# Performance work log

Hardware: AMD Instinct MI355X
Metric: run time of the kernel (lower is better)

Reference implementation:

```python
import jax, jax.numpy as jnp
import numpy as np

B, LQ, LK = 1, 2048, 2048
D, H, KVH, DH = 4096, 32, 8, 128
G = H // KVH  # head groups


def setup_inputs() -> dict:
    key = jax.random.key(0)
    ks = jax.random.split(key, 7)
    s = 0.02
    hidden_q = jax.random.normal(ks[0], (B, LQ, D), dtype=jnp.float32)
    hidden_kv = jax.random.normal(ks[1], (B, LK, D), dtype=jnp.float32)
    # causal boolean mask (batch, len_q, len_k)
    attention_mask = jnp.broadcast_to(jnp.tril(jnp.ones((LQ, LK), dtype=bool)), (B, LQ, LK))
    position_bias = jax.random.normal(ks[2], (H, LQ, LK), dtype=jnp.float32) * 0.1
    Wq = jax.random.normal(ks[3], (D, H * DH), dtype=jnp.float32) * s
    Wk = jax.random.normal(ks[4], (D, KVH * DH), dtype=jnp.float32) * s
    Wv = jax.random.normal(ks[5], (D, KVH * DH), dtype=jnp.float32) * s
    Wo = jax.random.normal(ks[6], (H * DH, D), dtype=jnp.float32) * s
    return {"hidden_q": hidden_q, "hidden_kv": hidden_kv,
            "attention_mask": attention_mask, "position_bias": position_bias,
            "Wq": Wq, "Wk": Wk, "Wv": Wv, "Wo": Wo}


def reference(hidden_q, hidden_kv, attention_mask, position_bias, Wq, Wk, Wv, Wo):
    inv4 = DH ** -0.25  # q and k each scaled by dim_head**-1/4
    q = (hidden_q @ Wq) * inv4            # [B, LQ, H*DH]
    k = (hidden_kv @ Wk) * inv4           # [B, LK, KVH*DH]
    v = hidden_kv @ Wv                     # [B, LK, KVH*DH]
    q = q.reshape(B, LQ, KVH, G, DH)       # group heads for GQA
    k = k.reshape(B, LK, KVH, DH)
    v = v.reshape(B, LK, KVH, DH)
    # score: [B, KVH, G, LQ, LK] -> [B, H, LQ, LK]
    score = jnp.einsum('bqkgd,blkd->bkgql', q, k).reshape(B, H, LQ, LK)
    score = score + position_bias[None]
    mask = attention_mask[:, None]         # [B, 1, LQ, LK]
    score = jnp.where(mask, score, -jnp.inf)
    p = jax.nn.softmax(score, axis=-1)
    p = jnp.where(mask, p, 0.0)
    out = jnp.einsum('bkgql,blkd->bqkgd', p.reshape(B, KVH, G, LQ, LK), v)
    out = out.reshape(B, LQ, H * DH) @ Wo  # [B, LQ, D]
    return out
```

## Files before the change

kernel.cpp:

```cpp
#include <hip/hip_runtime.h>
#include <hip/hip_bf16.h>
#include <cstdint>
#include <cstddef>

typedef __attribute__((ext_vector_type(4))) float f32x4;
typedef __attribute__((ext_vector_type(4))) short s16x4;
typedef __attribute__((ext_vector_type(8))) short s16x8;

#define SLQ 2048
#define SLK 2048
#define SNH 32
#define SDH 128
#define LOG2E 1.4426950408889634f

__device__ __forceinline__ short f2bf(float x) {
  unsigned u = __builtin_bit_cast(unsigned, x);
  u += 0x7FFF + ((u >> 16) & 1);
  return (short)(u >> 16);
}

__device__ __forceinline__ void gload_lds16(const void* g, const void* l) {
  __builtin_amdgcn_global_load_lds((const __attribute__((address_space(1))) void*)g,
                                   (__attribute__((address_space(3))) void*)l,
                                   16, 0, 0);
}

template<int CTRL>
__device__ __forceinline__ float dpp_f32(float x) {
  return __builtin_bit_cast(float, __builtin_amdgcn_update_dpp(
      0, __builtin_bit_cast(int, x), CTRL, 0xF, 0xF, true));
}
__device__ __forceinline__ float rowmax16(float x) {
  x = fmaxf(x, dpp_f32<0x128>(x));
  x = fmaxf(x, dpp_f32<0x124>(x));
  x = fmaxf(x, dpp_f32<0x122>(x));
  x = fmaxf(x, dpp_f32<0x121>(x));
  return x;
}
__device__ __forceinline__ float rowsum16(float x) {
  x += dpp_f32<0x128>(x);
  x += dpp_f32<0x124>(x);
  x += dpp_f32<0x122>(x);
  x += dpp_f32<0x121>(x);
  return x;
}

__global__ void convert_bf16_2(const float* __restrict__ in0, short* __restrict__ out0,
                               const float* __restrict__ in1, short* __restrict__ out1) {
  const int i = blockIdx.x * 256 + threadIdx.x;
  const float* in = blockIdx.y ? in1 : in0;
  short* out = blockIdx.y ? out1 : out0;
  f32x4 a = ((const f32x4*)in)[i];
  s16x4 b;
  b[0] = f2bf(a[0]); b[1] = f2bf(a[1]); b[2] = f2bf(a[2]); b[3] = f2bf(a[3]);
  ((s16x4*)out)[i] = b;
}

__global__ void transpose_all(const float* __restrict__ Wq, const float* __restrict__ Wo,
                              const float* __restrict__ Wk, const float* __restrict__ Wv,
                              short* __restrict__ WqT, short* __restrict__ WoT,
                              short* __restrict__ WkT, short* __restrict__ WvT) {
  __shared__ short T[64][68];
  const int K = 4096;
  int bx = blockIdx.x;
  const float* W; short* Wt; int N;
  if (bx < 64)       { W = Wq; Wt = WqT; N = 4096; }
  else if (bx < 128) { W = Wo; Wt = WoT; N = 4096; bx -= 64; }
  else if (bx < 144) { W = Wk; Wt = WkT; N = 1024; bx -= 128; }
  else               { W = Wv; Wt = WvT; N = 1024; bx -= 144; }
  const int tid = threadIdx.x;
  const int k0 = blockIdx.y * 64, n0 = bx * 64;
  const int r = tid >> 4;
  const int c4 = (tid & 15) * 4;
#pragma unroll
  for (int i = 0; i < 4; ++i) {
    f32x4 a = *(const f32x4*)(W + (size_t)(k0 + r + i * 16) * N + n0 + c4);
#pragma unroll
    for (int j = 0; j < 4; ++j) T[c4 + j][r + i * 16] = f2bf(a[j]);
  }
  __syncthreads();
  const int rn = tid >> 3;
  const int c8 = (tid & 7) * 8;
#pragma unroll
  for (int i = 0; i < 2; ++i) {
    s16x4 v0 = *(const s16x4*)&T[rn + i * 32][c8];
    s16x4 v1 = *(const s16x4*)&T[rn + i * 32][c8 + 4];
    short* dst = Wt + (size_t)(n0 + rn + i * 32) * K + k0 + c8;
    *(s16x4*)dst = v0;
    *(s16x4*)(dst + 4) = v1;
  }
}

template<int CM>
__global__ __launch_bounds__(512, 1)
void gemm_big(const short* __restrict__ A, const short* __restrict__ Bt,
              void* __restrict__ Cv, float scale) {
  __shared__ short As[3][128 * 64];
  __shared__ short Bs[3][256 * 64];
  const int N = 4096, K = 4096;
  const int tid = threadIdx.x, lane = tid & 63, w = tid >> 6;
  const int l15 = lane & 15, lg = lane >> 4;
  const int wr = w >> 2, wc = w & 3;
  const int nbx = N >> 8;
  const int nwg = gridDim.x, b = blockIdx.x;
  const int wg = (b & 7) * (nwg >> 3) + (b >> 3);
  const int m0 = (wg / nbx) * 128, n0 = (wg % nbx) * 256;

  f32x4 acc[4][4];
#pragma unroll
  for (int a = 0; a < 4; ++a)
#pragma unroll
    for (int c = 0; c < 4; ++c)
      acc[a][c] = (f32x4){0.f, 0.f, 0.f, 0.f};

#define GSTAGE(T, BUF) do {                                                    \
    _Pragma("unroll") for (int i_ = 0; i_ < 2; ++i_) {                         \
      const int ci = i_ * 512 + tid, r_ = ci >> 3, c_ = ci & 7;                \
      gload_lds16(A + (size_t)(m0 + r_) * K + (T) * 64 + ((c_ ^ (r_ & 7)) * 8),\
                  (const short*)As[BUF] + ci * 8); }                           \
    _Pragma("unroll") for (int i_ = 0; i_ < 4; ++i_) {                         \
      const int ci = i_ * 512 + tid, r_ = ci >> 3, c_ = ci & 7;                \
      gload_lds16(Bt + (size_t)(n0 + r_) * K + (T) * 64 + ((c_ ^ (r_ & 7)) * 8),\
                  (const short*)Bs[BUF] + ci * 8); }                           \
  } while (0)

  const int NT = K >> 6;
  GSTAGE(0, 0); GSTAGE(1, 1); GSTAGE(2, 2);
  int buf = 0;
  for (int t = 0; t < NT; ++t) {
    if (t + 2 < NT)      asm volatile("s_waitcnt vmcnt(12)" ::: "memory");
    else if (t + 1 < NT) asm volatile("s_waitcnt vmcnt(6)" ::: "memory");
    else                 asm volatile("s_waitcnt vmcnt(0)" ::: "memory");
    __builtin_amdgcn_s_barrier();
    const short* Ab = As[buf];
    const short* Bb = Bs[buf];
    s16x8 af[2][4], bfv[2][4];
#pragma unroll
    for (int kk = 0; kk < 2; ++kk) {
#pragma unroll
      for (int mi = 0; mi < 4; ++mi) {
        const int r = wr * 64 + mi * 16 + l15;
        const int c = (kk * 4 + lg) ^ (r & 7);
        af[kk][mi] = *(const s16x8*)(Ab + (r * 8 + c) * 8);
      }
#pragma unroll
      for (int ni = 0; ni < 4; ++ni) {
        const int r = wc * 64 + ni * 16 + l15;
        const int c = (kk * 4 + lg) ^ (r & 7);
        bfv[kk][ni] = *(const s16x8*)(Bb + (r * 8 + c) * 8);
      }
    }
    __builtin_amdgcn_s_setprio(1);
#pragma unroll
    for (int kk = 0; kk < 2; ++kk)
#pragma unroll
      for (int mi = 0; mi < 4; ++mi)
#pragma unroll
        for (int ni = 0; ni < 4; ++ni)
          acc[mi][ni] = __builtin_amdgcn_mfma_f32_16x16x32_bf16(af[kk][mi], bfv[kk][ni], acc[mi][ni], 0, 0, 0);
    __builtin_amdgcn_s_setprio(0);
    __builtin_amdgcn_s_barrier();
    if (t + 3 < NT) GSTAGE(t + 3, buf);
    buf = (buf == 2) ? 0 : buf + 1;
  }
#undef GSTAGE
#pragma unroll
  for (int mi = 0; mi < 4; ++mi) {
#pragma unroll
    for (int ni = 0; ni < 4; ++ni) {
#pragma unroll
      for (int j = 0; j < 4; ++j) {
        const int rg = m0 + wr * 64 + mi * 16 + lg * 4 + j;
        const int cg = n0 + wc * 64 + ni * 16 + l15;
        const float vv = acc[mi][ni][j] * scale;
        if (CM == 0) ((short*)Cv)[(size_t)rg * N + cg] = f2bf(vv);
        else         ((float*)Cv)[(size_t)rg * N + cg] = vv;
      }
    }
  }
}

__global__ __launch_bounds__(256, 2)
void gemm_kv(const short* __restrict__ A, const short* __restrict__ Bt,
             short* __restrict__ kout, short* __restrict__ vTout, float inv4) {
  __shared__ short As[128][32];
  __shared__ short Bs[128][32];
  const int N = 2048, K = 4096;
  const int tid = threadIdx.x, lane = tid & 63, wid = tid >> 6;
  const int l15 = lane & 15, lg = lane >> 4;
  const int nbx = N >> 7;
  const int nwg = gridDim.x, b = blockIdx.x;
  const int wg = (b & 7) * (nwg >> 3) + (b >> 3);
  const int m0 = (wg / nbx) * 128, n0 = (wg % nbx) * 128;
  const int wm = (wid >> 1) * 64, wn = (wid & 1) * 64;

  f32x4 acc[4][4];
#pragma unroll
  for (int a = 0; a < 4; ++a)
#pragma unroll
    for (int c = 0; c < 4; ++c)
      acc[a][c] = (f32x4){0.f, 0.f, 0.f, 0.f};

  for (int k0 = 0; k0 < K; k0 += 32) {
#pragma unroll
    for (int i = 0; i < 2; ++i) {
      const int c = i * 256 + wid * 64 + lane;
      const int rr = c >> 2, hh = (c & 3) * 8;
      gload_lds16(A  + (size_t)(m0 + rr) * K + k0 + hh,
                  (const short*)As + (size_t)(i * 256 + wid * 64) * 8);
      gload_lds16(Bt + (size_t)(n0 + rr) * K + k0 + hh,
                  (const short*)Bs + (size_t)(i * 256 + wid * 64) * 8);
    }
    __syncthreads();
    s16x8 af[4], bf[4];
#pragma unroll
    for (int mi = 0; mi < 4; ++mi)
      af[mi] = *(const s16x8*)&As[wm + mi * 16 + l15][lg * 8];
#pragma unroll
    for (int ni = 0; ni < 4; ++ni)
      bf[ni] = *(const s16x8*)&Bs[wn + ni * 16 + l15][lg * 8];
#pragma unroll
    for (int mi = 0; mi < 4; ++mi)
#pragma unroll
      for (int ni = 0; ni < 4; ++ni)
        acc[mi][ni] = __builtin_amdgcn_mfma_f32_16x16x32_bf16(af[mi], bf[ni], acc[mi][ni], 0, 0, 0);
    __syncthreads();
  }
  if (n0 < 1024) {
#pragma unroll
    for (int mi = 0; mi < 4; ++mi)
#pragma unroll
      for (int ni = 0; ni < 4; ++ni)
#pragma unroll
        for (int j = 0; j < 4; ++j) {
          const int rg = m0 + wm + mi * 16 + lg * 4 + j;
          const int cg = n0 + wn + ni * 16 + l15;
          kout[(size_t)rg * 1024 + cg] = f2bf(acc[mi][ni][j] * inv4);
        }
  } else {
#pragma unroll
    for (int mi = 0; mi < 4; ++mi)
#pragma unroll
      for (int ni = 0; ni < 4; ++ni) {
        s16x4 wv;
#pragma unroll
        for (int j = 0; j < 4; ++j) wv[j] = f2bf(acc[mi][ni][j]);
        const int rg0 = m0 + wm + mi * 16 + lg * 4;
        const int cg = n0 + wn + ni * 16 + l15 - 1024;
        *(s16x4*)(vTout + (size_t)cg * 2048 + rg0) = wv;
      }
  }
}

__global__ __launch_bounds__(256, 2)
void attn_kernel(const short* __restrict__ q, const short* __restrict__ k,
                 const short* __restrict__ vT, const float* __restrict__ bias,
                 short* __restrict__ o) {
  __shared__ __align__(16) short Ks[2][64 * 128];
  __shared__ __align__(16) short Vs[2][128 * 64];
  __shared__ __align__(16) short Ps[4][16][72];
  const int tid = threadIdx.x, lane = tid & 63, w = tid >> 6;
  const int l15 = lane & 15, lg = lane >> 4;
  const int b = blockIdx.x;
  const int h = b & 31;
  const int qt = 31 - (b >> 5);
  const int kvh = h >> 2;
  const int nt = qt + 1;

#define STAGE_K(IT, P) do { const int kv0_ = (IT) * 64;                       \
    _Pragma("unroll") for (int i_ = 0; i_ < 4; ++i_) {                        \
      const int ci = i_ * 256 + tid, r_ = ci >> 4, c_ = ci & 15;              \
      gload_lds16(k + (size_t)(kv0_ + r_) * 1024 + kvh * 128 + ((c_ ^ (r_ & 7)) * 8), \
                  (const short*)Ks[P] + ci * 8); } } while (0)

#define STAGE_V(IT, P) do { const int kv0_ = (IT) * 64;                       \
    _Pragma("unroll") for (int i_ = 0; i_ < 4; ++i_) {                        \
      const int ci = i_ * 256 + tid, r_ = ci >> 3, c_ = ci & 7;               \
      gload_lds16(vT + (size_t)(kvh * 128 + r_) * 2048 + kv0_ + ((c_ ^ (r_ & 7)) * 8), \
                  (const short*)Vs[P] + ci * 8); } } while (0)

  const int qrow0 = qt * 64 + w * 16 + lg * 4;

  float bb[4][4];
#define LOAD_BIAS(IT) do { const float* bp_ = bias + ((size_t)h * SLQ + qrow0) * SLK + (IT) * 64 + l15; \
    _Pragma("unroll") for (int ni_ = 0; ni_ < 4; ++ni_)                       \
      _Pragma("unroll") for (int j_ = 0; j_ < 4; ++j_)                        \
        bb[ni_][j_] = bp_[(size_t)j_ * SLK + ni_ * 16]; } while (0)

  s16x8 qf[4];
  {
    const short* qp = q + (size_t)(qt * 64 + w * 16 + l15) * (SNH * SDH) + h * SDH + lg * 8;
#pragma unroll
    for (int kk = 0; kk < 4; ++kk) qf[kk] = *(const s16x8*)(qp + kk * 32);
  }
  float mrow[4], lrow[4];
  f32x4 oacc[8];
#pragma unroll
  for (int j = 0; j < 4; ++j) { mrow[j] = -1e30f; lrow[j] = 0.f; }
#pragma unroll
  for (int nd = 0; nd < 8; ++nd) oacc[nd] = (f32x4){0.f, 0.f, 0.f, 0.f};

  STAGE_V(0, 0);
  STAGE_K(0, 0);
  LOAD_BIAS(0);

  for (int it = 0; it < nt; ++it) {
    const int p = it & 1;
    const int kv0 = it * 64;
    asm volatile("s_waitcnt vmcnt(16)" ::: "memory");
    __builtin_amdgcn_s_barrier();
    if (it + 1 < nt) { STAGE_V(it + 1, p ^ 1); STAGE_K(it + 1, p ^ 1); }
    f32x4 s[4];
    __builtin_amdgcn_s_setprio(1);
#pragma unroll
    for (int ni = 0; ni < 4; ++ni) {
      s[ni] = (f32x4){0.f, 0.f, 0.f, 0.f};
      const int r = ni * 16 + l15;
#pragma unroll
      for (int kk = 0; kk < 4; ++kk) {
        const int cc = kk * 4 + lg;
        s16x8 kf = *(const s16x8*)(Ks[p] + (r * 16 + (cc ^ (r & 7))) * 8);
        s[ni] = __builtin_amdgcn_mfma_f32_16x16x32_bf16(qf[kk], kf, s[ni], 0, 0, 0);
      }
    }
    __builtin_amdgcn_s_setprio(0);
#pragma unroll
    for (int ni = 0; ni < 4; ++ni) {
#pragma unroll
      for (int j = 0; j < 4; ++j) {
        float sv = fmaf(bb[ni][j], LOG2E, s[ni][j]);
        if (it == qt && kv0 + ni * 16 + l15 > qrow0 + j) sv = -1e30f;
        s[ni][j] = sv;
      }
    }
    if (it + 1 < nt) LOAD_BIAS(it + 1);
    float pmax[4];
#pragma unroll
    for (int j = 0; j < 4; ++j) {
      float mx = fmaxf(fmaxf(s[0][j], s[1][j]), fmaxf(s[2][j], s[3][j]));
      pmax[j] = rowmax16(mx);
    }
    bool need = (pmax[0] > mrow[0] + 11.54f) | (pmax[1] > mrow[1] + 11.54f) |
                (pmax[2] > mrow[2] + 11.54f) | (pmax[3] > mrow[3] + 11.54f);
    if (__any(need)) {
#pragma unroll
      for (int j = 0; j < 4; ++j) {
        const float mn = fmaxf(mrow[j], pmax[j]);
        const float fsj = exp2f(mrow[j] - mn);
        mrow[j] = mn;
        lrow[j] *= fsj;
#pragma unroll
        for (int nd = 0; nd < 8; ++nd) oacc[nd][j] *= fsj;
      }
    }
    float ps[4] = {0.f, 0.f, 0.f, 0.f};
#pragma unroll
    for (int ni = 0; ni < 4; ++ni)
#pragma unroll
      for (int j = 0; j < 4; ++j) {
        const float pv = exp2f(s[ni][j] - mrow[j]);
        s[ni][j] = pv;
        ps[j] += pv;
      }
#pragma unroll
    for (int j = 0; j < 4; ++j) lrow[j] += rowsum16(ps[j]);
#pragma unroll
    for (int ni = 0; ni < 4; ++ni)
#pragma unroll
      for (int j = 0; j < 4; ++j)
        Ps[w][lg * 4 + j][ni * 16 + l15] = f2bf(s[ni][j]);
    __builtin_amdgcn_s_setprio(1);
#pragma unroll
    for (int kk2 = 0; kk2 < 2; ++kk2) {
      s16x8 pa = *(const s16x8*)&Ps[w][l15][kk2 * 32 + lg * 8];
#pragma unroll
      for (int nd = 0; nd < 8; ++nd) {
        const int r = nd * 16 + l15;
        const int cc = kk2 * 4 + lg;
        s16x8 vf = *(const s16x8*)(Vs[p] + (r * 8 + (cc ^ (r & 7))) * 8);
        oacc[nd] = __builtin_amdgcn_mfma_f32_16x16x32_bf16(pa, vf, oacc[nd], 0, 0, 0);
      }
    }
    __builtin_amdgcn_s_setprio(0);
  }
#undef STAGE_K
#undef STAGE_V
#undef LOAD_BIAS
#pragma unroll
  for (int j = 0; j < 4; ++j) {
    const float inv = 1.f / lrow[j];
    short* op = o + (size_t)(qrow0 + j) * (SNH * SDH) + h * SDH + l15;
#pragma unroll
    for (int nd = 0; nd < 8; ++nd)
      op[nd * 16] = f2bf(oacc[nd][j] * inv);
  }
}

extern "C" void kernel_launch(void* const* d_in, const int* in_sizes, int n_in,
                              void* d_out, int out_size, void* d_ws, size_t ws_size,
                              hipStream_t stream) {
  (void)in_sizes; (void)n_in; (void)out_size; (void)ws_size;
  const float* hq   = (const float*)d_in[0];
  const float* hkv  = (const float*)d_in[1];
  const float* bias = (const float*)d_in[3];
  const float* Wq   = (const float*)d_in[4];
  const float* Wk   = (const float*)d_in[5];
  const float* Wv   = (const float*)d_in[6];
  const float* Wo   = (const float*)d_in[7];

  short* ws = (short*)d_ws;
  const size_t MEG = 1048576;
  short* hqb  = ws;
  short* hkvb = ws + 8 * MEG;
  short* WT   = ws + 16 * MEG;
  short* WoT  = ws + 32 * MEG;
  short* WkvT = ws + 48 * MEG;
  short* qb   = ws + 56 * MEG;
  short* kb   = ws + 64 * MEG;
  short* vbT  = ws + 66 * MEG;
  short* ob   = hqb;

  const float inv4 = 0.29730177875068026f;

  convert_bf16_2<<<dim3(8192, 2), 256, 0, stream>>>(hq, hqb, hkv, hkvb);
  transpose_all<<<dim3(160, 64), 256, 0, stream>>>(
      Wq, Wo, Wk, Wv, WT, WoT, WkvT, WkvT + (size_t)1024 * 4096);

  gemm_big<0><<<256, 512, 0, stream>>>(hqb, WT, qb, inv4 * LOG2E);
  gemm_kv<<<256, 256, 0, stream>>>(hkvb, WkvT, kb, vbT, inv4);

  attn_kernel<<<1024, 256, 0, stream>>>(qb, kb, vbT, bias, ob);

  gemm_big<1><<<256, 512, 0, stream>>>(ob, WoT, (float*)d_out, 1.0f);
}
```

Baseline: 473.1 us.

## Stage bias tiles through LDS and single-buffer K with split staging

Replaces per-thread strided global bias loads held in registers with asynchronous global-to-LDS staging of each 64x64 bias tile into a swizzled shared buffer. K becomes single-buffered and is staged together with bias after the softmax barrier, while V stays double-buffered, with the vmcnt waits adjusted to match. The softmax switches from exp2 with log2e folded into Q to natural __expf with a lower rescale threshold, dropping one FMA per score. The aim is fewer register-held bias loads and better-coalesced bias traffic, at the cost of an extra barrier per iteration and less prefetch distance for K and bias.

Result: faster. 462.2 us (-2.3%).

```diff
diff --git a/kernel.cpp b/kernel.cpp
--- a/kernel.cpp
+++ b/kernel.cpp
@@ -11,7 +11,6 @@
 #define SLK 2048
 #define SNH 32
 #define SDH 128
-#define LOG2E 1.4426950408889634f
 
 __device__ __forceinline__ short f2bf(float x) {
   unsigned u = __builtin_bit_cast(unsigned, x);
@@ -256,8 +255,9 @@
 void attn_kernel(const short* __restrict__ q, const short* __restrict__ k,
                  const short* __restrict__ vT, const float* __restrict__ bias,
                  short* __restrict__ o) {
-  __shared__ __align__(16) short Ks[2][64 * 128];
+  __shared__ __align__(16) short Ks[64 * 128];
   __shared__ __align__(16) short Vs[2][128 * 64];
+  __shared__ __align__(16) float Bb[64 * 64];
   __shared__ __align__(16) short Ps[4][16][72];
   const int tid = threadIdx.x, lane = tid & 63, w = tid >> 6;
   const int l15 = lane & 15, lg = lane >> 4;
@@ -267,11 +267,11 @@
   const int kvh = h >> 2;
   const int nt = qt + 1;
 
-#define STAGE_K(IT, P) do { const int kv0_ = (IT) * 64;                       \
+#define STAGE_K(IT) do { const int kv0_ = (IT) * 64;                          \
     _Pragma("unroll") for (int i_ = 0; i_ < 4; ++i_) {                        \
       const int ci = i_ * 256 + tid, r_ = ci >> 4, c_ = ci & 15;              \
       gload_lds16(k + (size_t)(kv0_ + r_) * 1024 + kvh * 128 + ((c_ ^ (r_ & 7)) * 8), \
-                  (const short*)Ks[P] + ci * 8); } } while (0)
+                  (const short*)Ks + ci * 8); } } while (0)
 
 #define STAGE_V(IT, P) do { const int kv0_ = (IT) * 64;                       \
     _Pragma("unroll") for (int i_ = 0; i_ < 4; ++i_) {                        \
@@ -279,13 +279,13 @@
       gload_lds16(vT + (size_t)(kvh * 128 + r_) * 2048 + kv0_ + ((c_ ^ (r_ & 7)) * 8), \
                   (const short*)Vs[P] + ci * 8); } } while (0)
 
+#define STAGE_B(IT) do { const int kv0_ = (IT) * 64;                          \
+    _Pragma("unroll") for (int i_ = 0; i_ < 4; ++i_) {                        \
+      const int ci = i_ * 256 + tid, r_ = ci >> 4, c_ = ci & 15;              \
+      gload_lds16(bias + ((size_t)h * SLQ + qt * 64 + r_) * SLK + kv0_ + ((c_ ^ (r_ & 7)) * 4), \
+                  (const float*)Bb + ci * 4); } } while (0)
+
   const int qrow0 = qt * 64 + w * 16 + lg * 4;
-
-  float bb[4][4];
-#define LOAD_BIAS(IT) do { const float* bp_ = bias + ((size_t)h * SLQ + qrow0) * SLK + (IT) * 64 + l15; \
-    _Pragma("unroll") for (int ni_ = 0; ni_ < 4; ++ni_)                       \
-      _Pragma("unroll") for (int j_ = 0; j_ < 4; ++j_)                        \
-        bb[ni_][j_] = bp_[(size_t)j_ * SLK + ni_ * 16]; } while (0)
 
   s16x8 qf[4];
   {
@@ -301,15 +301,15 @@
   for (int nd = 0; nd < 8; ++nd) oacc[nd] = (f32x4){0.f, 0.f, 0.f, 0.f};
 
   STAGE_V(0, 0);
-  STAGE_K(0, 0);
-  LOAD_BIAS(0);
+  STAGE_K(0);
+  STAGE_B(0);
 
   for (int it = 0; it < nt; ++it) {
     const int p = it & 1;
     const int kv0 = it * 64;
-    asm volatile("s_waitcnt vmcnt(16)" ::: "memory");
+    asm volatile("s_waitcnt vmcnt(4)" ::: "memory");
     __builtin_amdgcn_s_barrier();
-    if (it + 1 < nt) { STAGE_V(it + 1, p ^ 1); STAGE_K(it + 1, p ^ 1); }
+    if (it + 1 < nt) STAGE_V(it + 1, p ^ 1);
     f32x4 s[4];
     __builtin_amdgcn_s_setprio(1);
 #pragma unroll
@@ -319,34 +319,37 @@
 #pragma unroll
       for (int kk = 0; kk < 4; ++kk) {
         const int cc = kk * 4 + lg;
-        s16x8 kf = *(const s16x8*)(Ks[p] + (r * 16 + (cc ^ (r & 7))) * 8);
+        s16x8 kf = *(const s16x8*)(Ks + (r * 16 + (cc ^ (r & 7))) * 8);
         s[ni] = __builtin_amdgcn_mfma_f32_16x16x32_bf16(qf[kk], kf, s[ni], 0, 0, 0);
       }
     }
     __builtin_amdgcn_s_setprio(0);
+    if (it + 1 < nt) asm volatile("s_waitcnt vmcnt(4)" ::: "memory");
+    else             asm volatile("s_waitcnt vmcnt(0)" ::: "memory");
 #pragma unroll
     for (int ni = 0; ni < 4; ++ni) {
 #pragma unroll
       for (int j = 0; j < 4; ++j) {
-        float sv = fmaf(bb[ni][j], LOG2E, s[ni][j]);
+        const int rr = w * 16 + lg * 4 + j;
+        const int ch = (ni * 4 + (l15 >> 2)) ^ (rr & 7);
+        float sv = s[ni][j] + Bb[rr * 64 + ch * 4 + (l15 & 3)];
         if (it == qt && kv0 + ni * 16 + l15 > qrow0 + j) sv = -1e30f;
         s[ni][j] = sv;
       }
     }
-    if (it + 1 < nt) LOAD_BIAS(it + 1);
     float pmax[4];
 #pragma unroll
     for (int j = 0; j < 4; ++j) {
       float mx = fmaxf(fmaxf(s[0][j], s[1][j]), fmaxf(s[2][j], s[3][j]));
       pmax[j] = rowmax16(mx);
     }
-    bool need = (pmax[0] > mrow[0] + 11.54f) | (pmax[1] > mrow[1] + 11.54f) |
-                (pmax[2] > mrow[2] + 11.54f) | (pmax[3] > mrow[3] + 11.54f);
+    bool need = (pmax[0] > mrow[0] + 8.f) | (pmax[1] > mrow[1] + 8.f) |
+                (pmax[2] > mrow[2] + 8.f) | (pmax[3] > mrow[3] + 8.f);
     if (__any(need)) {
 #pragma unroll
       for (int j = 0; j < 4; ++j) {
         const float mn = fmaxf(mrow[j], pmax[j]);
-        const float fsj = exp2f(mrow[j] - mn);
+        const float fsj = __expf(mrow[j] - mn);
         mrow[j] = mn;
         lrow[j] *= fsj;
 #pragma unroll
@@ -358,12 +361,14 @@
     for (int ni = 0; ni < 4; ++ni)
 #pragma unroll
       for (int j = 0; j < 4; ++j) {
-        const float pv = exp2f(s[ni][j] - mrow[j]);
+        const float pv = __expf(s[ni][j] - mrow[j]);
         s[ni][j] = pv;
         ps[j] += pv;
       }
 #pragma unroll
     for (int j = 0; j < 4; ++j) lrow[j] += rowsum16(ps[j]);
+    __builtin_amdgcn_s_barrier();
+    if (it + 1 < nt) { STAGE_K(it + 1); STAGE_B(it + 1); }
 #pragma unroll
     for (int ni = 0; ni < 4; ++ni)
 #pragma unroll
@@ -385,7 +390,7 @@
   }
 #undef STAGE_K
 #undef STAGE_V
-#undef LOAD_BIAS
+#undef STAGE_B
 #pragma unroll
   for (int j = 0; j < 4; ++j) {
     const float inv = 1.f / lrow[j];
@@ -426,7 +431,7 @@
   transpose_all<<<dim3(160, 64), 256, 0, stream>>>(
       Wq, Wo, Wk, Wv, WT, WoT, WkvT, WkvT + (size_t)1024 * 4096);
 
-  gemm_big<0><<<256, 512, 0, stream>>>(hqb, WT, qb, inv4 * LOG2E);
+  gemm_big<0><<<256, 512, 0, stream>>>(hqb, WT, qb, inv4);
   gemm_kv<<<256, 256, 0, stream>>>(hkvb, WkvT, kb, vbT, inv4);
 
   attn_kernel<<<1024, 256, 0, stream>>>(qb, kb, vbT, bias, ob);
```

## Single-buffer K tile, double-buffer bias two iterations ahead, switch to natural exp

Applied to the files above, without the earlier changes.

The attention kernel now keeps a single K buffer in LDS and stages the next K tile after the QK phase, behind an extra barrier. Bias is prefetched two iterations ahead into two alternating register sets through a manually unrolled loop body. The log2e prescale is dropped: Q is no longer scaled by log2e, bias is added directly, __expf replaces exp2f, and the lazy-rescale threshold changes from 11.54 to 8. The aim is to cut LDS use for higher occupancy and to hide bias load latency, at the cost of an extra barrier per iteration, more registers, and a possibly costlier __expf.

Result: no change. 472.7 us (-0.1%).

```diff
diff --git a/kernel.cpp b/kernel.cpp
--- a/kernel.cpp
+++ b/kernel.cpp
@@ -11,7 +11,6 @@
 #define SLK 2048
 #define SNH 32
 #define SDH 128
-#define LOG2E 1.4426950408889634f
 
 __device__ __forceinline__ short f2bf(float x) {
   unsigned u = __builtin_bit_cast(unsigned, x);
@@ -256,7 +255,7 @@
 void attn_kernel(const short* __restrict__ q, const short* __restrict__ k,
                  const short* __restrict__ vT, const float* __restrict__ bias,
                  short* __restrict__ o) {
-  __shared__ __align__(16) short Ks[2][64 * 128];
+  __shared__ __align__(16) short Ks[64 * 128];
   __shared__ __align__(16) short Vs[2][128 * 64];
   __shared__ __align__(16) short Ps[4][16][72];
   const int tid = threadIdx.x, lane = tid & 63, w = tid >> 6;
@@ -267,11 +266,11 @@
   const int kvh = h >> 2;
   const int nt = qt + 1;
 
-#define STAGE_K(IT, P) do { const int kv0_ = (IT) * 64;                       \
+#define STAGE_K(IT) do { const int kv0_ = (IT) * 64;                          \
     _Pragma("unroll") for (int i_ = 0; i_ < 4; ++i_) {                        \
       const int ci = i_ * 256 + tid, r_ = ci >> 4, c_ = ci & 15;              \
       gload_lds16(k + (size_t)(kv0_ + r_) * 1024 + kvh * 128 + ((c_ ^ (r_ & 7)) * 8), \
-                  (const short*)Ks[P] + ci * 8); } } while (0)
+                  (const short*)Ks + ci * 8); } } while (0)
 
 #define STAGE_V(IT, P) do { const int kv0_ = (IT) * 64;                       \
     _Pragma("unroll") for (int i_ = 0; i_ < 4; ++i_) {                        \
@@ -281,11 +280,10 @@
 
   const int qrow0 = qt * 64 + w * 16 + lg * 4;
 
-  float bb[4][4];
-#define LOAD_BIAS(IT) do { const float* bp_ = bias + ((size_t)h * SLQ + qrow0) * SLK + (IT) * 64 + l15; \
+#define LOAD_BIAS(IT, BB) do { const float* bp_ = bias + ((size_t)h * SLQ + qrow0) * SLK + (IT) * 64 + l15; \
     _Pragma("unroll") for (int ni_ = 0; ni_ < 4; ++ni_)                       \
       _Pragma("unroll") for (int j_ = 0; j_ < 4; ++j_)                        \
-        bb[ni_][j_] = bp_[(size_t)j_ * SLK + ni_ * 16]; } while (0)
+        BB[ni_][j_] = bp_[(size_t)j_ * SLK + ni_ * 16]; } while (0)
 
   s16x8 qf[4];
   {
@@ -300,92 +298,92 @@
 #pragma unroll
   for (int nd = 0; nd < 8; ++nd) oacc[nd] = (f32x4){0.f, 0.f, 0.f, 0.f};
 
+  float bbA[4][4], bbB[4][4];
+
   STAGE_V(0, 0);
-  STAGE_K(0, 0);
-  LOAD_BIAS(0);
-
-  for (int it = 0; it < nt; ++it) {
-    const int p = it & 1;
-    const int kv0 = it * 64;
-    asm volatile("s_waitcnt vmcnt(16)" ::: "memory");
-    __builtin_amdgcn_s_barrier();
-    if (it + 1 < nt) { STAGE_V(it + 1, p ^ 1); STAGE_K(it + 1, p ^ 1); }
-    f32x4 s[4];
-    __builtin_amdgcn_s_setprio(1);
-#pragma unroll
-    for (int ni = 0; ni < 4; ++ni) {
-      s[ni] = (f32x4){0.f, 0.f, 0.f, 0.f};
-      const int r = ni * 16 + l15;
-#pragma unroll
-      for (int kk = 0; kk < 4; ++kk) {
-        const int cc = kk * 4 + lg;
-        s16x8 kf = *(const s16x8*)(Ks[p] + (r * 16 + (cc ^ (r & 7))) * 8);
-        s[ni] = __builtin_amdgcn_mfma_f32_16x16x32_bf16(qf[kk], kf, s[ni], 0, 0, 0);
-      }
-    }
-    __builtin_amdgcn_s_setprio(0);
-#pragma unroll
-    for (int ni = 0; ni < 4; ++ni) {
-#pragma unroll
-      for (int j = 0; j < 4; ++j) {
-        float sv = fmaf(bb[ni][j], LOG2E, s[ni][j]);
-        if (it == qt && kv0 + ni * 16 + l15 > qrow0 + j) sv = -1e30f;
-        s[ni][j] = sv;
-      }
-    }
-    if (it + 1 < nt) LOAD_BIAS(it + 1);
-    float pmax[4];
-#pragma unroll
-    for (int j = 0; j < 4; ++j) {
-      float mx = fmaxf(fmaxf(s[0][j], s[1][j]), fmaxf(s[2][j], s[3][j]));
-      pmax[j] = rowmax16(mx);
-    }
-    bool need = (pmax[0] > mrow[0] + 11.54f) | (pmax[1] > mrow[1] + 11.54f) |
-                (pmax[2] > mrow[2] + 11.54f) | (pmax[3] > mrow[3] + 11.54f);
-    if (__any(need)) {
-#pragma unroll
-      for (int j = 0; j < 4; ++j) {
-        const float mn = fmaxf(mrow[j], pmax[j]);
-        const float fsj = exp2f(mrow[j] - mn);
-        mrow[j] = mn;
-        lrow[j] *= fsj;
-#pragma unroll
-        for (int nd = 0; nd < 8; ++nd) oacc[nd][j] *= fsj;
-      }
-    }
-    float ps[4] = {0.f, 0.f, 0.f, 0.f};
-#pragma unroll
-    for (int ni = 0; ni < 4; ++ni)
-#pragma unroll
-      for (int j = 0; j < 4; ++j) {
-        const float pv = exp2f(s[ni][j] - mrow[j]);
-        s[ni][j] = pv;
-        ps[j] += pv;
-      }
-#pragma unroll
-    for (int j = 0; j < 4; ++j) lrow[j] += rowsum16(ps[j]);
-#pragma unroll
-    for (int ni = 0; ni < 4; ++ni)
-#pragma unroll
-      for (int j = 0; j < 4; ++j)
-        Ps[w][lg * 4 + j][ni * 16 + l15] = f2bf(s[ni][j]);
-    __builtin_amdgcn_s_setprio(1);
-#pragma unroll
-    for (int kk2 = 0; kk2 < 2; ++kk2) {
-      s16x8 pa = *(const s16x8*)&Ps[w][l15][kk2 * 32 + lg * 8];
-#pragma unroll
-      for (int nd = 0; nd < 8; ++nd) {
-        const int r = nd * 16 + l15;
-        const int cc = kk2 * 4 + lg;
-        s16x8 vf = *(const s16x8*)(Vs[p] + (r * 8 + (cc ^ (r & 7))) * 8);
-        oacc[nd] = __builtin_amdgcn_mfma_f32_16x16x32_bf16(pa, vf, oacc[nd], 0, 0, 0);
-      }
-    }
-    __builtin_amdgcn_s_setprio(0);
-  }
+  STAGE_K(0);
+  LOAD_BIAS(0, bbA);
+  if (nt > 1) LOAD_BIAS(1, bbB);
+
+#define BODY(IT, BB) do {                                                     \
+    const int p_ = (IT) & 1;                                                  \
+    const int kv0_ = (IT) * 64;                                               \
+    if ((IT) + 1 < nt) asm volatile("s_waitcnt vmcnt(16)" ::: "memory");      \
+    else               asm volatile("s_waitcnt vmcnt(0)"  ::: "memory");      \
+    __builtin_amdgcn_s_barrier();                                             \
+    if ((IT) + 1 < nt) STAGE_V((IT) + 1, p_ ^ 1);                             \
+    f32x4 s[4];                                                               \
+    __builtin_amdgcn_s_setprio(1);                                            \
+    _Pragma("unroll") for (int ni = 0; ni < 4; ++ni) {                        \
+      s[ni] = (f32x4){0.f, 0.f, 0.f, 0.f};                                    \
+      const int r = ni * 16 + l15;                                            \
+      _Pragma("unroll") for (int kk = 0; kk < 4; ++kk) {                      \
+        const int cc = kk * 4 + lg;                                           \
+        s16x8 kf = *(const s16x8*)(Ks + (r * 16 + (cc ^ (r & 7))) * 8);       \
+        s[ni] = __builtin_amdgcn_mfma_f32_16x16x32_bf16(qf[kk], kf, s[ni], 0, 0, 0); \
+      }                                                                       \
+    }                                                                         \
+    __builtin_amdgcn_s_setprio(0);                                            \
+    _Pragma("unroll") for (int ni = 0; ni < 4; ++ni) {                        \
+      _Pragma("unroll") for (int j = 0; j < 4; ++j) {                         \
+        float sv = s[ni][j] + BB[ni][j];                                      \
+        if ((IT) == qt && kv0_ + ni * 16 + l15 > qrow0 + j) sv = -1e30f;      \
+        s[ni][j] = sv;                                                        \
+      }                                                                       \
+    }                                                                         \
+    float pmax[4];                                                            \
+    _Pragma("unroll") for (int j = 0; j < 4; ++j) {                           \
+      float mx = fmaxf(fmaxf(s[0][j], s[1][j]), fmaxf(s[2][j], s[3][j]));     \
+      pmax[j] = rowmax16(mx);                                                 \
+    }                                                                         \
+    bool need = (pmax[0] > mrow[0] + 8.f) | (pmax[1] > mrow[1] + 8.f) |       \
+                (pmax[2] > mrow[2] + 8.f) | (pmax[3] > mrow[3] + 8.f);        \
+    if (__any(need)) {                                                        \
+      _Pragma("unroll") for (int j = 0; j < 4; ++j) {                         \
+        const float mn = fmaxf(mrow[j], pmax[j]);                             \
+        const float fsj = __expf(mrow[j] - mn);                               \
+        mrow[j] = mn;                                                         \
+        lrow[j] *= fsj;                                                       \
+        _Pragma("unroll") for (int nd = 0; nd < 8; ++nd) oacc[nd][j] *= fsj;  \
+      }                                                                       \
+    }                                                                         \
+    float ps[4] = {0.f, 0.f, 0.f, 0.f};                                       \
+    _Pragma("unroll") for (int ni = 0; ni < 4; ++ni)                          \
+      _Pragma("unroll") for (int j = 0; j < 4; ++j) {                         \
+        const float pv = __expf(s[ni][j] - mrow[j]);                          \
+        s[ni][j] = pv;                                                        \
+        ps[j] += pv;                                                          \
+      }                                                                       \
+    _Pragma("unroll") for (int j = 0; j < 4; ++j) lrow[j] += rowsum16(ps[j]); \
+    __builtin_amdgcn_s_barrier();                                             \
+    if ((IT) + 1 < nt) STAGE_K((IT) + 1);                                     \
+    if ((IT) + 2 < nt) LOAD_BIAS((IT) + 2, BB);                               \
+    _Pragma("unroll") for (int ni = 0; ni < 4; ++ni)                          \
+      _Pragma("unroll") for (int j = 0; j < 4; ++j)                           \
+        Ps[w][lg * 4 + j][ni * 16 + l15] = f2bf(s[ni][j]);                    \
+    __builtin_amdgcn_s_setprio(1);                                            \
+    _Pragma("unroll") for (int kk2 = 0; kk2 < 2; ++kk2) {                     \
+      s16x8 pa = *(const s16x8*)&Ps[w][l15][kk2 * 32 + lg * 8];               \
+      _Pragma("unroll") for (int nd = 0; nd < 8; ++nd) {                      \
+        const int r = nd * 16 + l15;                                          \
+        const int cc = kk2 * 4 + lg;                                          \
+        s16x8 vf = *(const s16x8*)(Vs[p_] + (r * 8 + (cc ^ (r & 7))) * 8);    \
+        oacc[nd] = __builtin_amdgcn_mfma_f32_16x16x32_bf16(pa, vf, oacc[nd], 0, 0, 0); \
+      }                                                                       \
+    }                                                                         \
+    __builtin_amdgcn_s_setprio(0);                                            \
+  } while (0)
+
+  for (int it = 0; it < nt; ) {
+    BODY(it, bbA);
+    ++it;
+    if (it < nt) { BODY(it, bbB); ++it; }
+  }
+#undef BODY
 #undef STAGE_K
 #undef STAGE_V
 #undef LOAD_BIAS
+
 #pragma unroll
   for (int j = 0; j < 4; ++j) {
     const float inv = 1.f / lrow[j];
@@ -426,7 +424,7 @@
   transpose_all<<<dim3(160, 64), 256, 0, stream>>>(
       Wq, Wo, Wk, Wv, WT, WoT, WkvT, WkvT + (size_t)1024 * 4096);
 
-  gemm_big<0><<<256, 512, 0, stream>>>(hqb, WT, qb, inv4 * LOG2E);
+  gemm_big<0><<<256, 512, 0, stream>>>(hqb, WT, qb, inv4);
   gemm_kv<<<256, 256, 0, stream>>>(hkvb, WkvT, kb, vbT, inv4);
 
   attn_kernel<<<1024, 256, 0, stream>>>(qb, kb, vbT, bias, ob);
```
